# Performance work log

Hardware: AMD Instinct MI355X
Metric: run time of the kernel (lower is better)

Reference implementation:

```python
import jax, jax.numpy as jnp
import numpy as np

NEG_INF = -1e9


def _rotate_half(x):
    h = x.shape[-1] // 2
    return jnp.concatenate([-x[..., h:], x[..., :h]], axis=-1)


def setup_inputs() -> dict:
    key = jax.random.key(0)
    ks = jax.random.split(key, 6)
    V, P, D, H = 4, 2048, 1280, 16
    hd = D // H
    return {
        "hidden_states": jax.random.normal(ks[0], (V, P, D), jnp.float32),
        "rope_cache": jax.random.normal(ks[1], (V, P, 1, 2 * hd), jnp.float32),
        "valid_lens": jax.random.randint(ks[2], (V,), 0, P, jnp.int32),
        "w_qkv": jax.random.normal(ks[3], (D, 3 * D), jnp.float32) * (D ** -0.5),
        "b_qkv": jnp.zeros((3 * D,), jnp.float32),
        "w_proj": jax.random.normal(ks[4], (D, D), jnp.float32) * (D ** -0.5),
        "b_proj": jnp.zeros((D,), jnp.float32),
        "n_heads": 16,
    }


def reference(hidden_states, rope_cache, valid_lens, w_qkv, b_qkv, w_proj, b_proj, n_heads):
    V, P, D = hidden_states.shape
    H = n_heads
    hd = D // H
    # fused QKV: (V, P, 3, H, hd)
    qkv = (hidden_states @ w_qkv + b_qkv).reshape(V, P, 3, H, hd)
    q, k, v = qkv[:, :, 0], qkv[:, :, 1], qkv[:, :, 2]  # each (V, P, H, hd)
    # 2D RoPE via precomputed cos/sin cache (V, P, 1, 2*hd)
    cos = rope_cache[..., :hd]
    sin = rope_cache[..., hd:]
    q = q * cos + _rotate_half(q) * sin
    k = k * cos + _rotate_half(k) * sin
    # attention with per-vision key padding mask (BlockMask equivalent)
    scale = hd ** -0.5
    scores = jnp.einsum("vqhd,vkhd->vhqk", q, k) * scale
    lens = jnp.maximum(valid_lens, 1)
    key_mask = jnp.arange(P)[None, :] < lens[:, None]  # (V, P)
    scores = jnp.where(key_mask[:, None, None, :], scores, NEG_INF)
    attn = jax.nn.softmax(scores, axis=-1)
    out = jnp.einsum("vhqk,vkhd->vqhd", attn, v).reshape(V, P, D)
    return out @ w_proj + b_proj
```

## Files before the change

kernel.cpp:

```cpp
#include <hip/hip_runtime.h>

typedef unsigned short u16;
typedef short bf16x8 __attribute__((ext_vector_type(8)));
typedef float f32x4 __attribute__((ext_vector_type(4)));

#define DEV __device__ __forceinline__

DEV float b2f(u16 u) { union { unsigned i; float f; } x; x.i = ((unsigned)u) << 16; return x.f; }
DEV u16 f2b(float f) {
  union { float f; unsigned i; } x; x.f = f;
  unsigned r = x.i + 0x7fffu + ((x.i >> 16) & 1u);
  return (u16)(r >> 16);
}

DEV float exp2g(float x) { return __builtin_amdgcn_exp2f(x); }

template<int CTRL>
DEV float dppmax(float x) {
  int t = __builtin_amdgcn_update_dpp(__builtin_bit_cast(int, x),
                                      __builtin_bit_cast(int, x), CTRL, 0xf, 0xf, false);
  return fmaxf(x, __builtin_bit_cast(float, t));
}

#define GLDS(gp, lp) __builtin_amdgcn_global_load_lds( \
    (const __attribute__((address_space(1))) void*)(gp), \
    (__attribute__((address_space(3))) void*)(lp), 16, 0, 0)

constexpr float QSCALE = 0.11180339887498949f * 1.4426950408889634f;

__global__ __launch_bounds__(256) void prep_k(const float* __restrict__ hidden,
    u16* __restrict__ Ah, const float* __restrict__ wq, u16* __restrict__ Btq)
{
  __shared__ u16 tile[64 * 40];
  int b = blockIdx.x, tid = threadIdx.x;
  if (b < 5120) {
    int i = (b * 256 + tid) * 8;
    f32x4 a = *(const f32x4*)(hidden + i);
    f32x4 c = *(const f32x4*)(hidden + i + 4);
    bf16x8 o;
#pragma unroll
    for (int j = 0; j < 4; ++j) { o[j] = (short)f2b(a[j]); o[4 + j] = (short)f2b(c[j]); }
    *(bf16x8*)(Ah + i) = o;
  } else {
    int tb = b - 5120;
    int bx = tb % 60, by = tb / 60;
    const int Kd = 1280, Nd = 3840;
    int k0 = by * 32, n0 = bx * 64;
#pragma unroll
    for (int t = 0; t < 2; ++t) {
      int c = t * 256 + tid;
      int k_l = c >> 4, n_l = (c & 15) << 2;
      f32x4 vv = *(const f32x4*)(wq + (size_t)(k0 + k_l) * Nd + n0 + n_l);
#pragma unroll
      for (int j = 0; j < 4; ++j) tile[(n_l + j) * 40 + k_l] = f2b(vv[j]);
    }
    __syncthreads();
    int n_l = tid >> 2, kc = (tid & 3) << 3;
    bf16x8 vv = *(const bf16x8*)(tile + n_l * 40 + kc);
    *(bf16x8*)(Btq + (size_t)(n0 + n_l) * Kd + k0 + kc) = vv;
  }
}

template<int MODE>
__global__ __launch_bounds__(256) void gemm_k(const u16* __restrict__ A,
    const u16* __restrict__ Bt, const float* __restrict__ bias,
    u16* __restrict__ Oq, u16* __restrict__ Ok, u16* __restrict__ Ov,
    float* __restrict__ Of, const int* __restrict__ lens, int M, int N, int K)
{
  __shared__ u16 Asm[128 * 64];
  __shared__ u16 Bsm[128 * 64];
  const int tid = threadIdx.x;
  const int w = tid >> 6, lane = tid & 63, quad = lane >> 4, l16 = lane & 15;
  const int wm = w >> 1, wn = w & 1;
  const int m0 = blockIdx.y * 128, n0 = blockIdx.x * 128;

  if (MODE == 0) {
    if (n0 >= 1280) {
      int vv = m0 >> 11, p0 = m0 & 2047;
      int len = lens[vv]; if (len < 1) len = 1;
      if (p0 >= len) return;
    }
  }

  const int srow = tid >> 3, spc = tid & 7;

  const f32x4 zero4 = {0.f, 0.f, 0.f, 0.f};
  f32x4 acc[4][4];
#pragma unroll
  for (int i = 0; i < 4; ++i)
#pragma unroll
    for (int j = 0; j < 4; ++j) acc[i][j] = zero4;

  for (int k0 = 0; k0 < K; k0 += 64) {
    __syncthreads();
#pragma unroll
    for (int g = 0; g < 4; ++g) {
      int r = g * 32 + srow;
      int q = spc ^ (r & 7);
      GLDS(A + (size_t)(m0 + r) * K + k0 + q * 8, Asm + r * 64 + spc * 8);
      GLDS(Bt + (size_t)(n0 + r) * K + k0 + q * 8, Bsm + r * 64 + spc * 8);
    }
    __syncthreads();
#pragma unroll
    for (int ks = 0; ks < 2; ++ks) {
      bf16x8 af[4], bfr[4];
#pragma unroll
      for (int mi = 0; mi < 4; ++mi) {
        int lr = wm * 64 + mi * 16 + l16;
        int ph = (ks * 4 + quad) ^ (lr & 7);
        af[mi] = *(const bf16x8*)(Asm + lr * 64 + ph * 8);
      }
#pragma unroll
      for (int ni = 0; ni < 4; ++ni) {
        int nr = wn * 64 + ni * 16 + l16;
        int ph = (ks * 4 + quad) ^ (nr & 7);
        bfr[ni] = *(const bf16x8*)(Bsm + nr * 64 + ph * 8);
      }
#pragma unroll
      for (int mi = 0; mi < 4; ++mi)
#pragma unroll
        for (int ni = 0; ni < 4; ++ni)
          acc[mi][ni] = __builtin_amdgcn_mfma_f32_16x16x32_bf16(af[mi], bfr[ni], acc[mi][ni], 0, 0, 0);
    }
  }

#pragma unroll
  for (int mi = 0; mi < 4; ++mi) {
#pragma unroll
    for (int ni = 0; ni < 4; ++ni) {
      int n = n0 + wn * 64 + ni * 16 + l16;
      float bb = bias[n];
#pragma unroll
      for (int r = 0; r < 4; ++r) {
        int m = m0 + wm * 64 + mi * 16 + quad * 4 + r;
        float val = acc[mi][ni][r] + bb;
        if (MODE == 0) {
          int t = n / 1280, rr = n - t * 1280;
          int hh = rr / 80, dd = rr - hh * 80;
          int vv = m >> 11, p = m & 2047;
          int vh = vv * 16 + hh;
          if (t == 0)      Oq[(size_t)(vh * 2048 + p) * 80 + dd] = f2b(val);
          else if (t == 1) Ok[(size_t)(vh * 2048 + p) * 80 + dd] = f2b(val);
          else             Ov[((size_t)vh * 80 + dd) * 2048 + p] = f2b(val);
        } else {
          Of[(size_t)m * N + n] = val;
        }
      }
    }
  }
}

__global__ __launch_bounds__(256) void rope_proj_k(u16* __restrict__ Q, u16* __restrict__ K,
    const float* __restrict__ rope, const float* __restrict__ wp, u16* __restrict__ Btp)
{
  __shared__ u16 tile[64 * 40];
  int b = blockIdx.x, tid = threadIdx.x;
  if (b < 5120) {
    int idx = b * 256 + tid;
    int which = idx >= 655360 ? 1 : 0;
    int r = which ? idx - 655360 : idx;
    int row = r / 5, c = r - row * 5;
    int d0 = c * 8;
    int p = row & 2047, vv = row >> 15;
    u16* buf = which ? K : Q;
    size_t base = (size_t)row * 80;
    int rc = (vv * 2048 + p) * 160;
    bf16x8 x0 = *(const bf16x8*)(buf + base + d0);
    bf16x8 x1 = *(const bf16x8*)(buf + base + 40 + d0);
    f32x4 c0a = *(const f32x4*)(rope + rc + d0);
    f32x4 c0b = *(const f32x4*)(rope + rc + d0 + 4);
    f32x4 c1a = *(const f32x4*)(rope + rc + 40 + d0);
    f32x4 c1b = *(const f32x4*)(rope + rc + 44 + d0);
    f32x4 s0a = *(const f32x4*)(rope + rc + 80 + d0);
    f32x4 s0b = *(const f32x4*)(rope + rc + 84 + d0);
    f32x4 s1a = *(const f32x4*)(rope + rc + 120 + d0);
    f32x4 s1b = *(const f32x4*)(rope + rc + 124 + d0);
    float sc = which ? 1.0f : QSCALE;
    bf16x8 y0, y1;
#pragma unroll
    for (int j = 0; j < 8; ++j) {
      float xa = b2f((u16)x0[j]), xb = b2f((u16)x1[j]);
      float cc0 = j < 4 ? c0a[j & 3] : c0b[j & 3];
      float cc1 = j < 4 ? c1a[j & 3] : c1b[j & 3];
      float ss0 = j < 4 ? s0a[j & 3] : s0b[j & 3];
      float ss1 = j < 4 ? s1a[j & 3] : s1b[j & 3];
      y0[j] = (short)f2b((xa * cc0 - xb * ss0) * sc);
      y1[j] = (short)f2b((xb * cc1 + xa * ss1) * sc);
    }
    *(bf16x8*)(buf + base + d0) = y0;
    *(bf16x8*)(buf + base + 40 + d0) = y1;
  } else {
    int tb = b - 5120;
    int bx = tb % 20, by = tb / 20;
    const int Kd = 1280, Nd = 1280;
    int k0 = by * 32, n0 = bx * 64;
#pragma unroll
    for (int t = 0; t < 2; ++t) {
      int c = t * 256 + tid;
      int k_l = c >> 4, n_l = (c & 15) << 2;
      f32x4 vv = *(const f32x4*)(wp + (size_t)(k0 + k_l) * Nd + n0 + n_l);
#pragma unroll
      for (int j = 0; j < 4; ++j) tile[(n_l + j) * 40 + k_l] = f2b(vv[j]);
    }
    __syncthreads();
    int n_l = tid >> 2, kc = (tid & 3) << 3;
    bf16x8 vv = *(const bf16x8*)(tile + n_l * 40 + kc);
    *(bf16x8*)(Btp + (size_t)(n0 + n_l) * Kd + k0 + kc) = vv;
  }
}

__global__ __launch_bounds__(256) void attn_k(const u16* __restrict__ Q,
    const u16* __restrict__ K, const u16* __restrict__ V,
    const int* __restrict__ lens, u16* __restrict__ O, const u16* __restrict__ zbuf)
{
  __shared__ u16 Ksm[64 * 96];
  __shared__ u16 Vt[96 * 64];
  __shared__ u16 Psm[4][16 * 72];
  const int v = blockIdx.z, h = blockIdx.y, q0 = blockIdx.x * 64;
  const int tid = threadIdx.x, w = tid >> 6, lane = tid & 63;
  const int quad = lane >> 4, l16 = lane & 15;
  int len = lens[v]; if (len < 1) len = 1;
  const int vh = v * 16 + h;

  if (tid < 128) {
    int row = 80 + (tid >> 3), pc = tid & 7;
    short val = (row == 80) ? (short)0x3F80 : (short)0;
    bf16x8 v8 = {val, val, val, val, val, val, val, val};
    *(bf16x8*)(Vt + row * 64 + pc * 8) = v8;
  }

  const bf16x8 zero8 = {0, 0, 0, 0, 0, 0, 0, 0};
  bf16x8 qf[3];
  {
    const u16* qp = Q + (size_t)(vh * 2048 + q0 + w * 16 + l16) * 80 + quad * 8;
    qf[0] = *(const bf16x8*)(qp);
    qf[1] = *(const bf16x8*)(qp + 32);
    qf[2] = (quad < 2) ? *(const bf16x8*)(qp + 64) : zero8;
  }

  const u16* kp[3]; int kstr[3];
#pragma unroll
  for (int t = 0; t < 3; ++t) {
    int L = w * 192 + t * 64 + lane;
    int key = L / 12, pc = L - key * 12;
    int q = (pc < 8) ? (pc ^ (key & 7)) : (8 + ((pc - 8) ^ (key & 3)));
    bool valid = q < 10;
    kp[t] = valid ? (K + (size_t)(vh * 2048 + key) * 80 + q * 8) : zbuf;
    kstr[t] = valid ? 5120 : 0;
  }
  const u16* vp[3];
  bool vok[3];
#pragma unroll
  for (int t = 0; t < 3; ++t) {
    int seg = w + t * 4;
    int d = seg * 8 + (lane >> 3), pc = lane & 7;
    int q = pc ^ (d & 7);
    vp[t] = V + ((size_t)vh * 80 + d) * 2048 + q * 8;
    vok[t] = seg < 10;
  }

  f32x4 kreg[3], vreg[3];
#define ISSUE_KV() do { \
  _Pragma("unroll") \
  for (int t = 0; t < 3; ++t) { kreg[t] = *(const f32x4*)(kp[t]); kp[t] += kstr[t]; } \
  _Pragma("unroll") \
  for (int t = 0; t < 3; ++t) { if (vok[t]) { vreg[t] = *(const f32x4*)(vp[t]); vp[t] += 64; } } \
} while (0)
#define WRITE_KV() do { \
  _Pragma("unroll") \
  for (int t = 0; t < 3; ++t) *(f32x4*)(Ksm + (w * 192 + t * 64 + lane) * 8) = kreg[t]; \
  _Pragma("unroll") \
  for (int t = 0; t < 3; ++t) { if (vok[t]) *(f32x4*)(Vt + (w + t * 4) * 512 + lane * 8) = vreg[t]; } \
} while (0)

  const f32x4 zero4 = {0.f, 0.f, 0.f, 0.f};
  f32x4 o[6];
#pragma unroll
  for (int i = 0; i < 6; ++i) o[i] = zero4;
  float m_run[4] = {-3e38f, -3e38f, -3e38f, -3e38f};

  ISSUE_KV();
  for (int key0 = 0; key0 < len; key0 += 64) {
    __syncthreads();
    WRITE_KV();
    __syncthreads();
    if (key0 + 64 < len) ISSUE_KV();

    f32x4 s[4];
#pragma unroll
    for (int i = 0; i < 4; ++i) s[i] = zero4;
    __builtin_amdgcn_s_setprio(1);
#pragma unroll
    for (int ks = 0; ks < 3; ++ks) {
      int ph = (ks < 2) ? ((ks * 4 + quad) ^ (l16 & 7)) : (8 + (quad ^ (l16 & 3)));
#pragma unroll
      for (int ni = 0; ni < 4; ++ni) {
        bf16x8 kb = *(const bf16x8*)(Ksm + (ni * 16 + l16) * 96 + ph * 8);
        s[ni] = __builtin_amdgcn_mfma_f32_16x16x32_bf16(qf[ks], kb, s[ni], 0, 0, 0);
      }
    }
    __builtin_amdgcn_s_setprio(0);

    if (key0 + 64 > len) {
#pragma unroll
      for (int ni = 0; ni < 4; ++ni) {
        int key = key0 + ni * 16 + l16;
        if (key >= len) {
#pragma unroll
          for (int r = 0; r < 4; ++r) s[ni][r] = -1e9f;
        }
      }
    }
    float mx[4];
#pragma unroll
    for (int r = 0; r < 4; ++r) {
      mx[r] = fmaxf(fmaxf(s[0][r], s[1][r]), fmaxf(s[2][r], s[3][r]));
      mx[r] = dppmax<0xB1>(mx[r]);
      mx[r] = dppmax<0x4E>(mx[r]);
      mx[r] = dppmax<0x124>(mx[r]);
      mx[r] = dppmax<0x128>(mx[r]);
    }

    int grow = (mx[0] > m_run[0] + 8.f) | (mx[1] > m_run[1] + 8.f) |
               (mx[2] > m_run[2] + 8.f) | (mx[3] > m_run[3] + 8.f);
    if (__any(grow)) {
      float alpha[4];
#pragma unroll
      for (int r = 0; r < 4; ++r) {
        float mn = fmaxf(m_run[r], mx[r]);
        alpha[r] = exp2g(m_run[r] - mn);
        m_run[r] = mn;
      }
#pragma unroll
      for (int ni = 0; ni < 6; ++ni)
#pragma unroll
        for (int r = 0; r < 4; ++r) o[ni][r] *= alpha[r];
    }

#pragma unroll
    for (int ni = 0; ni < 4; ++ni)
#pragma unroll
      for (int r = 0; r < 4; ++r) s[ni][r] = exp2g(s[ni][r] - m_run[r]);

#pragma unroll
    for (int ni = 0; ni < 4; ++ni) {
      unsigned w0, w1;
      asm("v_cvt_pk_bf16_f32 %0, %1, %2" : "=v"(w0) : "v"(s[ni][0]), "v"(s[ni][1]));
      asm("v_cvt_pk_bf16_f32 %0, %1, %2" : "=v"(w1) : "v"(s[ni][2]), "v"(s[ni][3]));
      u16* pp = &Psm[w][ni * 16 + l16];
      pp[(quad * 4 + 0) * 72] = (u16)w0;
      pp[(quad * 4 + 1) * 72] = (u16)(w0 >> 16);
      pp[(quad * 4 + 2) * 72] = (u16)w1;
      pp[(quad * 4 + 3) * 72] = (u16)(w1 >> 16);
    }

    __builtin_amdgcn_s_setprio(1);
#pragma unroll
    for (int ks = 0; ks < 2; ++ks) {
      bf16x8 pa = *(const bf16x8*)(&Psm[w][l16 * 72 + ks * 32 + quad * 8]);
      int ph = (ks * 4 + quad) ^ (l16 & 7);
#pragma unroll
      for (int ni = 0; ni < 6; ++ni) {
        bf16x8 vb = *(const bf16x8*)(Vt + (ni * 16 + l16) * 64 + ph * 8);
        o[ni] = __builtin_amdgcn_mfma_f32_16x16x32_bf16(pa, vb, o[ni], 0, 0, 0);
      }
    }
    __builtin_amdgcn_s_setprio(0);
  }
  float inv[4];
#pragma unroll
  for (int r = 0; r < 4; ++r) {
    float l = __shfl(o[5][r], (lane & 48), 64);
    inv[r] = 1.0f / l;
  }
#pragma unroll
  for (int ni = 0; ni < 5; ++ni)
#pragma unroll
    for (int r = 0; r < 4; ++r) {
      int qq = q0 + w * 16 + quad * 4 + r;
      O[((size_t)(v * 2048 + qq) * 16 + h) * 80 + ni * 16 + l16] = f2b(o[ni][r] * inv[r]);
    }
#undef ISSUE_KV
#undef WRITE_KV
}

extern "C" void kernel_launch(void* const* d_in, const int* in_sizes, int n_in,
                              void* d_out, int out_size, void* d_ws, size_t ws_size,
                              hipStream_t stream) {
  const float* hidden = (const float*)d_in[0];
  const float* rope   = (const float*)d_in[1];
  const int*   lens   = (const int*)d_in[2];
  const float* w_qkv  = (const float*)d_in[3];
  const float* b_qkv  = (const float*)d_in[4];
  const float* w_proj = (const float*)d_in[5];
  const float* b_proj = (const float*)d_in[6];
  float* out = (float*)d_out;
  char* ws = (char*)d_ws;
  u16* Ah = (u16*)(ws);
  u16* Bt = (u16*)(ws + 20971520);
  u16* Qb = (u16*)(ws + 30801920);
  u16* Kb = (u16*)(ws + 51773440);
  u16* Vb = (u16*)(ws + 72744960);
  u16* At = Ah;
  u16* Bp = Bt;

  prep_k<<<7520, 256, 0, stream>>>(hidden, Ah, w_qkv, Bt);
  gemm_k<0><<<dim3(30, 64), 256, 0, stream>>>(Ah, Bt, b_qkv, Qb, Kb, Vb, nullptr, lens, 8192, 3840, 1280);
  rope_proj_k<<<5920, 256, 0, stream>>>(Qb, Kb, rope, w_proj, Bp);
  attn_k<<<dim3(32, 16, 4), 256, 0, stream>>>(Qb, Kb, Vb, lens, At, (const u16*)b_qkv);
  gemm_k<1><<<dim3(10, 64), 256, 0, stream>>>(At, Bp, b_proj, nullptr, nullptr, nullptr, out, lens, 8192, 1280, 1280);
}
```

Measured before the change: 371.7 us.

## Rewrite attention with 32x32x16 MFMA, S^T layout and register-only P

```diff
diff --git a/kernel.cpp b/kernel.cpp
--- a/kernel.cpp
+++ b/kernel.cpp
@@ -3,6 +3,7 @@
 typedef unsigned short u16;
 typedef short bf16x8 __attribute__((ext_vector_type(8)));
 typedef float f32x4 __attribute__((ext_vector_type(4)));
+typedef float f32x16 __attribute__((ext_vector_type(16)));
 
 #define DEV __device__ __forceinline__
 
@@ -15,11 +16,13 @@
 
 DEV float exp2g(float x) { return __builtin_amdgcn_exp2f(x); }
 
-template<int CTRL>
-DEV float dppmax(float x) {
-  int t = __builtin_amdgcn_update_dpp(__builtin_bit_cast(int, x),
-                                      __builtin_bit_cast(int, x), CTRL, 0xf, 0xf, false);
-  return fmaxf(x, __builtin_bit_cast(float, t));
+DEV unsigned pk(float lo, float hi) {
+  unsigned r;
+  asm("v_cvt_pk_bf16_f32 %0, %1, %2" : "=v"(r) : "v"(lo), "v"(hi));
+  return r;
+}
+DEV void plswap(unsigned &a, unsigned &b) {
+  asm("v_permlane32_swap_b32 %0, %1" : "+v"(a), "+v"(b));
 }
 
 #define GLDS(gp, lp) __builtin_amdgcn_global_load_lds( \
@@ -215,27 +218,23 @@
 {
   __shared__ u16 Ksm[64 * 96];
   __shared__ u16 Vt[96 * 64];
-  __shared__ u16 Psm[4][16 * 72];
-  const int v = blockIdx.z, h = blockIdx.y, q0 = blockIdx.x * 64;
+  const int v = blockIdx.z, h_head = blockIdx.y, q0 = blockIdx.x * 128;
   const int tid = threadIdx.x, w = tid >> 6, lane = tid & 63;
-  const int quad = lane >> 4, l16 = lane & 15;
+  const int l32 = lane & 31, hh = lane >> 5;
   int len = lens[v]; if (len < 1) len = 1;
-  const int vh = v * 16 + h;
+  const int vh = v * 16 + h_head;
 
   if (tid < 128) {
     int row = 80 + (tid >> 3), pc = tid & 7;
-    short val = (row == 80) ? (short)0x3F80 : (short)0;
-    bf16x8 v8 = {val, val, val, val, val, val, val, val};
-    *(bf16x8*)(Vt + row * 64 + pc * 8) = v8;
-  }
-
-  const bf16x8 zero8 = {0, 0, 0, 0, 0, 0, 0, 0};
-  bf16x8 qf[3];
+    bf16x8 z8 = {0, 0, 0, 0, 0, 0, 0, 0};
+    *(bf16x8*)(Vt + row * 64 + pc * 8) = z8;
+  }
+
+  bf16x8 qf[5];
   {
-    const u16* qp = Q + (size_t)(vh * 2048 + q0 + w * 16 + l16) * 80 + quad * 8;
-    qf[0] = *(const bf16x8*)(qp);
-    qf[1] = *(const bf16x8*)(qp + 32);
-    qf[2] = (quad < 2) ? *(const bf16x8*)(qp + 64) : zero8;
+    const u16* qp = Q + (size_t)(vh * 2048 + q0 + w * 32 + l32) * 80 + hh * 8;
+#pragma unroll
+    for (int step = 0; step < 5; ++step) qf[step] = *(const bf16x8*)(qp + 16 * step);
   }
 
   const u16* kp[3]; int kstr[3];
@@ -273,113 +272,118 @@
   for (int t = 0; t < 3; ++t) { if (vok[t]) *(f32x4*)(Vt + (w + t * 4) * 512 + lane * 8) = vreg[t]; } \
 } while (0)
 
-  const f32x4 zero4 = {0.f, 0.f, 0.f, 0.f};
-  f32x4 o[6];
-#pragma unroll
-  for (int i = 0; i < 6; ++i) o[i] = zero4;
-  float m_run[4] = {-3e38f, -3e38f, -3e38f, -3e38f};
+  f32x16 o[3];
+#pragma unroll
+  for (int i = 0; i < 3; ++i)
+#pragma unroll
+    for (int r = 0; r < 16; ++r) o[i][r] = 0.f;
+  float m_run = -3e38f, l_run = 0.f;
 
   ISSUE_KV();
   for (int key0 = 0; key0 < len; key0 += 64) {
     __syncthreads();
     WRITE_KV();
-    __syncthreads();
     if (key0 + 64 < len) ISSUE_KV();
-
-    f32x4 s[4];
-#pragma unroll
-    for (int i = 0; i < 4; ++i) s[i] = zero4;
+    __syncthreads();
+
+    f32x16 s0, s1;
+#pragma unroll
+    for (int r = 0; r < 16; ++r) { s0[r] = 0.f; s1[r] = 0.f; }
     __builtin_amdgcn_s_setprio(1);
 #pragma unroll
-    for (int ks = 0; ks < 3; ++ks) {
-      int ph = (ks < 2) ? ((ks * 4 + quad) ^ (l16 & 7)) : (8 + (quad ^ (l16 & 3)));
-#pragma unroll
-      for (int ni = 0; ni < 4; ++ni) {
-        bf16x8 kb = *(const bf16x8*)(Ksm + (ni * 16 + l16) * 96 + ph * 8);
-        s[ni] = __builtin_amdgcn_mfma_f32_16x16x32_bf16(qf[ks], kb, s[ni], 0, 0, 0);
+    for (int step = 0; step < 5; ++step) {
+      int ph = (step < 4) ? ((2 * step + hh) ^ (l32 & 7)) : (8 + (hh ^ (l32 & 3)));
+      bf16x8 kb0 = *(const bf16x8*)(Ksm + l32 * 96 + ph * 8);
+      bf16x8 kb1 = *(const bf16x8*)(Ksm + (32 + l32) * 96 + ph * 8);
+      s0 = __builtin_amdgcn_mfma_f32_32x32x16_bf16(kb0, qf[step], s0, 0, 0, 0);
+      s1 = __builtin_amdgcn_mfma_f32_32x32x16_bf16(kb1, qf[step], s1, 0, 0, 0);
+    }
+    __builtin_amdgcn_s_setprio(0);
+
+    if (key0 + 64 > len) {
+      int thr = len - key0;
+#pragma unroll
+      for (int r = 0; r < 16; ++r) {
+        int c0 = (r & 3) + 8 * (r >> 2) + 4 * hh;
+        if (c0 >= thr) s0[r] = -1e9f;
+        if (32 + c0 >= thr) s1[r] = -1e9f;
       }
     }
+
+    float m8[8];
+#pragma unroll
+    for (int i = 0; i < 8; ++i)
+      m8[i] = fmaxf(fmaxf(s0[i], s0[i + 8]), fmaxf(s1[i], s1[i + 8]));
+    float m4a = fmaxf(m8[0], m8[4]), m4b = fmaxf(m8[1], m8[5]);
+    float m4c = fmaxf(m8[2], m8[6]), m4d = fmaxf(m8[3], m8[7]);
+    float mx = fmaxf(fmaxf(m4a, m4b), fmaxf(m4c, m4d));
+    mx = fmaxf(mx, __shfl_xor(mx, 32, 64));
+
+    int grow = mx > m_run + 8.f;
+    if (__any(grow)) {
+      float mn = fmaxf(m_run, mx);
+      float alpha = exp2g(m_run - mn);
+      m_run = mn;
+      l_run *= alpha;
+#pragma unroll
+      for (int r = 0; r < 16; ++r) {
+        float ar = __shfl(alpha, (r & 3) + 8 * (r >> 2) + 4 * hh, 64);
+        o[0][r] *= ar; o[1][r] *= ar; o[2][r] *= ar;
+      }
+    }
+
+#pragma unroll
+    for (int r = 0; r < 16; ++r) {
+      s0[r] = exp2g(s0[r] - m_run);
+      s1[r] = exp2g(s1[r] - m_run);
+    }
+
+    {
+      float a8[8];
+#pragma unroll
+      for (int i = 0; i < 8; ++i)
+        a8[i] = (s0[i] + s0[i + 8]) + (s1[i] + s1[i + 8]);
+      float ts = ((a8[0] + a8[4]) + (a8[1] + a8[5])) + ((a8[2] + a8[6]) + (a8[3] + a8[7]));
+      l_run += ts + __shfl_xor(ts, 32, 64);
+    }
+
+    __builtin_amdgcn_s_setprio(1);
+#define PVSTEP(SK, KS) do { \
+    unsigned A0 = pk(SK[((KS & 1) * 8) + 0], SK[((KS & 1) * 8) + 1]); \
+    unsigned A1 = pk(SK[((KS & 1) * 8) + 2], SK[((KS & 1) * 8) + 3]); \
+    unsigned B0 = pk(SK[((KS & 1) * 8) + 4], SK[((KS & 1) * 8) + 5]); \
+    unsigned B1 = pk(SK[((KS & 1) * 8) + 6], SK[((KS & 1) * 8) + 7]); \
+    plswap(A0, B0); plswap(A1, B1); \
+    union { unsigned u[4]; bf16x8 v8; } pu; \
+    pu.u[0] = A0; pu.u[1] = A1; pu.u[2] = B0; pu.u[3] = B1; \
+    int phv = (2 * (KS) + hh) ^ (l32 & 7); \
+    _Pragma("unroll") \
+    for (int ni = 0; ni < 3; ++ni) { \
+      bf16x8 vb = *(const bf16x8*)(Vt + (l32 + 32 * ni) * 64 + phv * 8); \
+      o[ni] = __builtin_amdgcn_mfma_f32_32x32x16_bf16(pu.v8, vb, o[ni], 0, 0, 0); \
+    } \
+  } while (0)
+    PVSTEP(s0, 0);
+    PVSTEP(s0, 1);
+    PVSTEP(s1, 2);
+    PVSTEP(s1, 3);
+#undef PVSTEP
     __builtin_amdgcn_s_setprio(0);
-
-    if (key0 + 64 > len) {
-#pragma unroll
-      for (int ni = 0; ni < 4; ++ni) {
-        int key = key0 + ni * 16 + l16;
-        if (key >= len) {
-#pragma unroll
-          for (int r = 0; r < 4; ++r) s[ni][r] = -1e9f;
-        }
-      }
-    }
-    float mx[4];
-#pragma unroll
-    for (int r = 0; r < 4; ++r) {
-      mx[r] = fmaxf(fmaxf(s[0][r], s[1][r]), fmaxf(s[2][r], s[3][r]));
-      mx[r] = dppmax<0xB1>(mx[r]);
-      mx[r] = dppmax<0x4E>(mx[r]);
-      mx[r] = dppmax<0x124>(mx[r]);
-      mx[r] = dppmax<0x128>(mx[r]);
-    }
-
-    int grow = (mx[0] > m_run[0] + 8.f) | (mx[1] > m_run[1] + 8.f) |
-               (mx[2] > m_run[2] + 8.f) | (mx[3] > m_run[3] + 8.f);
-    if (__any(grow)) {
-      float alpha[4];
-#pragma unroll
-      for (int r = 0; r < 4; ++r) {
-        float mn = fmaxf(m_run[r], mx[r]);
-        alpha[r] = exp2g(m_run[r] - mn);
-        m_run[r] = mn;
-      }
-#pragma unroll
-      for (int ni = 0; ni < 6; ++ni)
-#pragma unroll
-        for (int r = 0; r < 4; ++r) o[ni][r] *= alpha[r];
-    }
-
-#pragma unroll
-    for (int ni = 0; ni < 4; ++ni)
-#pragma unroll
-      for (int r = 0; r < 4; ++r) s[ni][r] = exp2g(s[ni][r] - m_run[r]);
-
-#pragma unroll
-    for (int ni = 0; ni < 4; ++ni) {
-      unsigned w0, w1;
-      asm("v_cvt_pk_bf16_f32 %0, %1, %2" : "=v"(w0) : "v"(s[ni][0]), "v"(s[ni][1]));
-      asm("v_cvt_pk_bf16_f32 %0, %1, %2" : "=v"(w1) : "v"(s[ni][2]), "v"(s[ni][3]));
-      u16* pp = &Psm[w][ni * 16 + l16];
-      pp[(quad * 4 + 0) * 72] = (u16)w0;
-      pp[(quad * 4 + 1) * 72] = (u16)(w0 >> 16);
-      pp[(quad * 4 + 2) * 72] = (u16)w1;
-      pp[(quad * 4 + 3) * 72] = (u16)(w1 >> 16);
-    }
-
-    __builtin_amdgcn_s_setprio(1);
-#pragma unroll
-    for (int ks = 0; ks < 2; ++ks) {
-      bf16x8 pa = *(const bf16x8*)(&Psm[w][l16 * 72 + ks * 32 + quad * 8]);
-      int ph = (ks * 4 + quad) ^ (l16 & 7);
-#pragma unroll
-      for (int ni = 0; ni < 6; ++ni) {
-        bf16x8 vb = *(const bf16x8*)(Vt + (ni * 16 + l16) * 64 + ph * 8);
-        o[ni] = __builtin_amdgcn_mfma_f32_16x16x32_bf16(pa, vb, o[ni], 0, 0, 0);
-      }
-    }
-    __builtin_amdgcn_s_setprio(0);
-  }
-  float inv[4];
-#pragma unroll
-  for (int r = 0; r < 4; ++r) {
-    float l = __shfl(o[5][r], (lane & 48), 64);
-    inv[r] = 1.0f / l;
-  }
-#pragma unroll
-  for (int ni = 0; ni < 5; ++ni)
-#pragma unroll
-    for (int r = 0; r < 4; ++r) {
-      int qq = q0 + w * 16 + quad * 4 + r;
-      O[((size_t)(v * 2048 + qq) * 16 + h) * 80 + ni * 16 + l16] = f2b(o[ni][r] * inv[r]);
-    }
+  }
+
+  float inv = 1.0f / l_run;
+#pragma unroll
+  for (int r = 0; r < 16; ++r) {
+    int rowc = (r & 3) + 8 * (r >> 2) + 4 * hh;
+    float ir = __shfl(inv, rowc, 64);
+    int qq = q0 + w * 32 + rowc;
+    size_t ob = ((size_t)(v * 2048 + qq) * 16 + h_head) * 80;
+#pragma unroll
+    for (int ni = 0; ni < 3; ++ni) {
+      int d = l32 + 32 * ni;
+      if (ni < 2 || l32 < 16) O[ob + d] = f2b(o[ni][r] * ir);
+    }
+  }
 #undef ISSUE_KV
 #undef WRITE_KV
 }
@@ -407,6 +411,6 @@
   prep_k<<<7520, 256, 0, stream>>>(hidden, Ah, w_qkv, Bt);
   gemm_k<0><<<dim3(30, 64), 256, 0, stream>>>(Ah, Bt, b_qkv, Qb, Kb, Vb, nullptr, lens, 8192, 3840, 1280);
   rope_proj_k<<<5920, 256, 0, stream>>>(Qb, Kb, rope, w_proj, Bp);
-  attn_k<<<dim3(32, 16, 4), 256, 0, stream>>>(Qb, Kb, Vb, lens, At, (const u16*)b_qkv);
+  attn_k<<<dim3(16, 16, 4), 256, 0, stream>>>(Qb, Kb, Vb, lens, At, (const u16*)b_qkv);
   gemm_k<1><<<dim3(10, 64), 256, 0, stream>>>(At, Bp, b_proj, nullptr, nullptr, nullptr, out, lens, 8192, 1280, 1280);
 }
```

Result: slower. 389.6 us (+4.8%).
